# Kernel tuning notes

Measured on AMD Instinct MI355X. Metric: run time of the kernel, lower is better.

The kernel has to match this reference:

```python
import jax, jax.numpy as jnp
import numpy as np

B, NE, DE = 4096, 64, 96
NA, NACT = 8, 16
DH, NH, OD = 256, 4, 64
HD = DH // NH


def setup_inputs() -> dict:
    key = jax.random.key(0)
    ks = jax.random.split(key, 16)
    s = 0.02
    entities = jax.random.normal(ks[0], (B, NE, DE), jnp.float32)
    entity_mask = jax.random.randint(ks[1], (B, NE), 0, 2, jnp.int32)
    obs_mask = jax.random.randint(ks[2], (B, NE, NE), 0, 2, jnp.int32)
    act_ids = jax.random.randint(ks[3], (B, NA), 0, NACT)
    actions_onehot = jax.nn.one_hot(act_ids, NACT, dtype=jnp.float32)
    return {
        "entities": entities,
        "entity_mask": entity_mask,
        "obs_mask": obs_mask,
        "actions_onehot": actions_onehot,
        "We": jax.random.normal(ks[4], (DE, DH), jnp.float32) * s,
        "be": jnp.zeros((DH,), jnp.float32),
        "Wa": jax.random.normal(ks[5], (NACT, DH), jnp.float32) * s,
        "Win": jax.random.normal(ks[6], (DH, 3 * DH), jnp.float32) * s,
        "Wout": jax.random.normal(ks[7], (DH, DH), jnp.float32) * s,
        "bout": jnp.zeros((DH,), jnp.float32),
        "Wm1": jax.random.normal(ks[8], (DH, DH), jnp.float32) * s,
        "bm1": jnp.zeros((DH,), jnp.float32),
        "Wm2": jax.random.normal(ks[9], (DH, OD), jnp.float32) * s,
        "bm2": jnp.zeros((OD,), jnp.float32),
        "Wl1": jax.random.normal(ks[10], (DH, DH), jnp.float32) * s,
        "bl1": jnp.zeros((DH,), jnp.float32),
        "Wl2": jax.random.normal(ks[11], (DH, OD), jnp.float32) * s,
        "bl2": jnp.zeros((OD,), jnp.float32),
    }


def reference(entities, entity_mask, obs_mask, actions_onehot,
              We, be, Wa, Win, Wout, bout,
              Wm1, bm1, Wm2, bm2, Wl1, bl1, Wl2, bl2):
    # entity encode + action embed, scattered into first NA entity slots
    he = entities @ We + be                      # [B, NE, DH]
    ha = actions_onehot @ Wa                     # [B, NA, DH]
    ha_pad = jnp.zeros_like(he).at[:, :NA].set(ha)
    x = jax.nn.relu(he + ha_pad)                 # [B, NE, DH]

    # multi-head attention: NA agent queries attend to NE entities
    qkv = x @ Win                                # [B, NE, 3*DH]
    q, k, v = jnp.split(qkv, 3, axis=-1)
    q = q[:, :NA].reshape(B, NA, NH, HD)
    k = k.reshape(B, NE, NH, HD)
    v = v.reshape(B, NE, NH, HD)
    logits = jnp.einsum('bqhd,bkhd->bhqk', q, k) / jnp.sqrt(jnp.float32(HD))
    pre = obs_mask[:, :NA, :NE].astype(bool)[:, None, :, :]  # [B,1,NA,NE]
    logits = jnp.where(pre, -jnp.inf, logits)
    w = jax.nn.softmax(logits, axis=-1)
    w = jnp.where(jnp.isnan(w), 0.0, w)          # fully-masked rows -> 0
    attn = jnp.einsum('bhqk,bkhd->bqhd', w, v).reshape(B, NA, DH)
    attn = attn @ Wout + bout
    post = entity_mask[:, :NA].astype(bool)[..., None]  # [B, NA, 1]
    hidden = jax.nn.relu(jnp.where(post, 0.0, attn))

    mean = jax.nn.relu(hidden @ Wm1 + bm1) @ Wm2 + bm2
    logvar = jnp.clip(jax.nn.relu(hidden @ Wl1 + bl1) @ Wl2 + bl2, -10.0, 0.0)
    return mean, logvar
```

## Files before the change

### kernel.cpp

```cpp
#include <hip/hip_runtime.h>
#include <hip/hip_bf16.h>
#include <math.h>

typedef __attribute__((ext_vector_type(8))) short short8;
typedef __attribute__((ext_vector_type(4))) float f32x4;
typedef __attribute__((ext_vector_type(2))) unsigned int uint2v;

#define DEVINL static __device__ __forceinline__

static constexpr int NBLK = 2048;

static constexpr int WE_OFF  = 0;
static constexpr int WQ_OFF  = 24576;
static constexpr int WKT_OFF = 90112;
static constexpr int WV_OFF  = 155648;
static constexpr int WO_OFF  = 221184;
static constexpr int WM1_OFF = 286720;
static constexpr int WM2_OFF = 352256;
static constexpr int WL1_OFF = 368640;
static constexpr int WL2_OFF = 434176;

static constexpr int XOFF   = 0;
static constexpr int WLOFF  = 0;
static constexpr int ATOFF  = 8192;
static constexpr int HOFF   = 16384;
static constexpr int M1OFF  = 24576;
static constexpr int L1OFF  = 32768;
static constexpr int XTOFF  = 65536;
static constexpr int EOFF   = 131072;
static constexpr int TOFF   = 131072;
static constexpr int WXOFF  = 131072;
static constexpr int ACTOFF = 155648;
static constexpr int QOFF   = 155648;
static constexpr int LDS_BYTES = 163840;

DEVINL unsigned short f2bf(float f) {
  union { float f; unsigned u; } x; x.f = f;
  unsigned r = x.u + 0x7fffu + ((x.u >> 16) & 1u);
  return (unsigned short)(r >> 16);
}

DEVINL f32x4 mfma(short8 a, short8 b, f32x4 c) {
  return __builtin_amdgcn_mfma_f32_16x16x32_bf16(a, b, c, 0, 0, 0);
}

DEVINL short8 ldfrag(const unsigned short* wf, int off, int nt, int kt, int nkt, int lane) {
  return *(const short8*)(wf + off + ((nt * nkt + kt) << 9) + (lane << 3));
}

__global__ __launch_bounds__(512) void prep_kernel(
    const float* We, const float* Win, const float* Wout, const float* Wm1,
    const float* Wm2, const float* Wl1, const float* Wl2, unsigned short* wf) {
  const int m = blockIdx.y;
  const int idx = blockIdx.x * 512 + threadIdx.x;
  if (m == 2) {
    if (idx >= 65536) return;
    const int h = idx >> 14, d = (idx >> 6) & 255, hd = idx & 63;
    const float v = Win[(long)d * 768 + 256 + h * 64 + hd];
    const int kt = hd >> 5, gg = (hd >> 3) & 3, j = hd & 7;
    wf[WKT_OFF + (((h * 16 + (d >> 4)) * 2 + kt) << 9) + (gg * 16 + (d & 15)) * 8 + j] =
        f2bf(v);
    return;
  }
  const int Ks[9]  = {96, 256, 0, 256, 256, 256, 256, 256, 256};
  const int Ns[9]  = {256, 256, 0, 256, 256, 256, 64, 256, 64};
  const int ld_[9] = {256, 768, 0, 768, 256, 256, 64, 256, 64};
  const int co_[9] = {0, 0, 0, 512, 0, 0, 0, 0, 0};
  const int off[9] = {WE_OFF, WQ_OFF, 0, WV_OFF, WO_OFF, WM1_OFF, WM2_OFF, WL1_OFF, WL2_OFF};
  const float* S[9] = {We, Win, Win, Win, Wout, Wm1, Wm2, Wl1, Wl2};
  const int K = Ks[m], N = Ns[m];
  if (idx >= K * N) return;
  const int row = idx / N, col = idx - row * N;
  const float v = S[m][(long)row * ld_[m] + co_[m] + col];
  const int nkt = K >> 5;
  wf[off[m] + ((((col >> 4) * nkt) + (row >> 5)) << 9) +
     ((((row >> 3) & 3) << 4) + (col & 15)) * 8 + (row & 7)] = f2bf(v);
}

__global__ __launch_bounds__(1024, 4) void fused_kernel(
    const float* __restrict__ entities, const int* __restrict__ entity_mask,
    const int* __restrict__ obs_mask, const float* __restrict__ acts,
    const float* __restrict__ Wa, const float* __restrict__ be,
    const float* __restrict__ bout, const float* __restrict__ bm1,
    const float* __restrict__ bm2, const float* __restrict__ bl1,
    const float* __restrict__ bl2, const unsigned short* __restrict__ wf,
    float* __restrict__ out) {
  extern __shared__ char sm[];
  const int tid = threadIdx.x;
  const int w = tid >> 6, lane = tid & 63;
  const int g = lane >> 4, c = lane & 15;
  const int ig0 = blockIdx.x * 2;

  {
    const int it = tid >> 9, i = tid & 511;
    const int row = i >> 3, seg = i & 7;
    const float* src = entities + (long)(ig0 + it) * 6144 + row * 96 + seg * 12;
    const int ebase = EOFF + it * 12288 + row * 192;
    const int sw = (row & 3) << 4;
#pragma unroll
    for (int p = 0; p < 3; ++p) {
      float4 f = *(const float4*)(src + p * 4);
      uint2v u;
      u.x = f2bf(f.x) | ((unsigned)f2bf(f.y) << 16);
      u.y = f2bf(f.z) | ((unsigned)f2bf(f.w) << 16);
      *(uint2v*)(sm + ebase + ((seg * 24 + p * 8) ^ sw)) = u;
    }
    if (tid < 16) {
      const float* oh = acts + ((long)(ig0 + (tid >> 3)) * 8 + (tid & 7)) * 16;
      int id = 0;
#pragma unroll
      for (int a = 0; a < 16; ++a) if (oh[a] > 0.5f) id = a;
      ((int*)(sm + ACTOFF))[tid] = id;
    }
  }
  __syncthreads();

  {
    f32x4 acc[2][4] = {};
#pragma unroll
    for (int kt = 0; kt < 3; ++kt) {
      short8 b = ldfrag(wf, WE_OFF, w, kt, 3, lane);
#pragma unroll
      for (int it = 0; it < 2; ++it)
#pragma unroll
        for (int mt = 0; mt < 4; ++mt) {
          const int row = mt * 16 + c;
          short8 a = *(const short8*)(sm + EOFF + it * 12288 + row * 192 +
                                      ((kt * 64 + g * 16) ^ ((row & 3) << 4)));
          acc[it][mt] = mfma(a, b, acc[it][mt]);
        }
    }
    const int col = w * 16 + c;
    const float bev = be[col];
#pragma unroll
    for (int it = 0; it < 2; ++it)
#pragma unroll
      for (int mt = 0; mt < 4; ++mt) {
        float vv[4];
#pragma unroll
        for (int r = 0; r < 4; ++r) {
          const int row = mt * 16 + g * 4 + r;
          float v = acc[it][mt][r] + bev;
          if (row < 8) {
            int id = ((const int*)(sm + ACTOFF))[it * 8 + row];
            v += Wa[id * 256 + col];
          }
          v = fmaxf(v, 0.f);
          vv[r] = v;
          *(unsigned short*)(sm + XOFF + it * 32768 + row * 512 +
                             ((col * 2) ^ ((row & 7) << 4))) = f2bf(v);
        }
        uint2v u;
        u.x = f2bf(vv[0]) | ((unsigned)f2bf(vv[1]) << 16);
        u.y = f2bf(vv[2]) | ((unsigned)f2bf(vv[3]) << 16);
        *(uint2v*)(sm + XTOFF + it * 32768 + col * 128 +
                   ((mt * 32 + g * 8) ^ ((col & 7) << 4))) = u;
      }
  }
  __syncthreads();

  {
    f32x4 qa = {0.f, 0.f, 0.f, 0.f};
#pragma unroll
    for (int kt = 0; kt < 8; ++kt) {
      short8 b = ldfrag(wf, WQ_OFF, w, kt, 8, lane);
      short8 a = *(const short8*)(sm + XOFF + (c >> 3) * 32768 + (c & 7) * 512 +
                                  ((kt * 64 + g * 16) ^ ((c & 7) << 4)));
      qa = mfma(a, b, qa);
    }
#pragma unroll
    for (int r = 0; r < 4; ++r) {
      const int qq = g * 4 + r;
      *(unsigned short*)(sm + QOFF + qq * 512 +
                         (((w * 16 + c) * 2) ^ ((qq & 7) << 4))) = f2bf(qa[r]);
    }
  }
  __syncthreads();

  {
    const int h = w >> 2, dq = w & 3;
    f32x4 ta[4] = {};
#pragma unroll
    for (int kt = 0; kt < 2; ++kt) {
      short8 a = *(const short8*)(sm + QOFF + c * 512 +
                                  ((h * 128 + kt * 64 + g * 16) ^ ((c & 7) << 4)));
#pragma unroll
      for (int n = 0; n < 4; ++n) {
        short8 b = ldfrag(wf, WKT_OFF, h * 16 + dq * 4 + n, kt, 2, lane);
        ta[n] = mfma(a, b, ta[n]);
      }
    }
    __syncthreads();
#pragma unroll
    for (int n = 0; n < 4; ++n)
#pragma unroll
      for (int r = 0; r < 4; ++r) {
        const int qq = g * 4 + r;
        const int col = (dq * 4 + n) * 16 + c;
        *(unsigned short*)(sm + TOFF + h * 8192 + qq * 512 +
                           ((col * 2) ^ ((qq & 7) << 4))) = f2bf(ta[n][r]);
      }
  }
  __syncthreads();

  {
    const int it = (w >> 2) & 1, h = w & 3;
    float wvals[4][4];
    f32x4 lac[4] = {};
    if (w < 8) {
#pragma unroll
      for (int kt = 0; kt < 8; ++kt) {
        short8 a = *(const short8*)(sm + TOFF + h * 8192 + (it * 8 + (c & 7)) * 512 +
                                    ((kt * 64 + g * 16) ^ ((c & 7) << 4)));
#pragma unroll
        for (int nt = 0; nt < 4; ++nt) {
          const int key = nt * 16 + c;
          short8 b = *(const short8*)(sm + XOFF + it * 32768 + key * 512 +
                                      ((kt * 64 + g * 16) ^ ((key & 7) << 4)));
          lac[nt] = mfma(a, b, lac[nt]);
        }
      }
      if (g < 2) {
        const int* obs = obs_mask + (long)(ig0 + it) * 4096;
#pragma unroll
        for (int r = 0; r < 4; ++r) {
          const int qi = g * 4 + r;
          float vals[4];
#pragma unroll
          for (int nt = 0; nt < 4; ++nt) {
            int msk = obs[qi * 64 + nt * 16 + c];
            vals[nt] = msk ? -INFINITY : lac[nt][r] * 0.125f;
          }
          float mx = fmaxf(fmaxf(vals[0], vals[1]), fmaxf(vals[2], vals[3]));
#pragma unroll
          for (int d = 1; d < 16; d <<= 1) mx = fmaxf(mx, __shfl_xor(mx, d, 64));
          float s = 0.f;
#pragma unroll
          for (int nt = 0; nt < 4; ++nt) {
            float e = (mx == -INFINITY) ? 0.f : expf(vals[nt] - mx);
            vals[nt] = e; s += e;
          }
#pragma unroll
          for (int d = 1; d < 16; d <<= 1) s += __shfl_xor(s, d, 64);
          const float inv = (s > 0.f) ? 1.f / s : 0.f;
#pragma unroll
          for (int nt = 0; nt < 4; ++nt) wvals[r][nt] = vals[nt] * inv;
        }
      }
    }
    __syncthreads();
    if (w < 8 && g < 2) {
#pragma unroll
      for (int r = 0; r < 4; ++r) {
        const int qi = g * 4 + r;
#pragma unroll
        for (int nt = 0; nt < 4; ++nt) {
          const int key = nt * 16 + c;
          *(unsigned short*)(sm + WLOFF + ((it * 4 + h) * 8 + qi) * 128 +
                             ((key * 2) ^ ((qi & 7) << 4))) = f2bf(wvals[r][nt]);
        }
      }
    }
  }
  __syncthreads();

  {
    const int it = w >> 3, h = (w >> 1) & 3, dh = w & 1;
    f32x4 xa[8] = {};
#pragma unroll
    for (int kt = 0; kt < 2; ++kt) {
      short8 a = *(const short8*)(sm + WLOFF + ((it * 4 + h) * 8 + (c & 7)) * 128 +
                                  ((kt * 64 + g * 16) ^ ((c & 7) << 4)));
#pragma unroll
      for (int n = 0; n < 8; ++n) {
        const int d = dh * 128 + n * 16 + c;
        short8 b = *(const short8*)(sm + XTOFF + it * 32768 + d * 128 +
                                    ((kt * 64 + g * 16) ^ ((d & 7) << 4)));
        xa[n] = mfma(a, b, xa[n]);
      }
    }
    if (g < 2) {
#pragma unroll
      for (int n = 0; n < 8; ++n)
#pragma unroll
        for (int r = 0; r < 4; ++r) {
          const int qq = it * 8 + g * 4 + r;
          const int col = h * 256 + dh * 128 + n * 16 + c;
          *(unsigned short*)(sm + WXOFF + qq * 2048 +
                             ((col * 2) ^ ((qq & 7) << 4))) = f2bf(xa[n][r]);
        }
    }
  }
  __syncthreads();

  {
    const int h = w >> 2, n = w & 3;
    f32x4 aac = {0.f, 0.f, 0.f, 0.f};
#pragma unroll
    for (int kt = 0; kt < 8; ++kt) {
      short8 a = *(const short8*)(sm + WXOFF + c * 2048 +
                                  ((h * 512 + kt * 64 + g * 16) ^ ((c & 7) << 4)));
      short8 b = ldfrag(wf, WV_OFF, h * 4 + n, kt, 8, lane);
      aac = mfma(a, b, aac);
    }
#pragma unroll
    for (int r = 0; r < 4; ++r) {
      const int qq = g * 4 + r;
      const int col = (h * 4 + n) * 16 + c;
      *(unsigned short*)(sm + ATOFF + qq * 512 +
                         ((col * 2) ^ ((qq & 7) << 4))) = f2bf(aac[r]);
    }
  }
  __syncthreads();

  {
    f32x4 hc = {0.f, 0.f, 0.f, 0.f};
#pragma unroll
    for (int kt = 0; kt < 8; ++kt) {
      short8 a = *(const short8*)(sm + ATOFF + c * 512 +
                                  ((kt * 64 + g * 16) ^ ((c & 7) << 4)));
      short8 b = ldfrag(wf, WO_OFF, w, kt, 8, lane);
      hc = mfma(a, b, hc);
    }
    const int col = w * 16 + c;
    const float bo = bout[col];
#pragma unroll
    for (int r = 0; r < 4; ++r) {
      const int qq = g * 4 + r;
      const int em = entity_mask[(long)(ig0 + (qq >> 3)) * 64 + (qq & 7)];
      float v = hc[r] + bo;
      v = em ? 0.f : fmaxf(v, 0.f);
      *(unsigned short*)(sm + HOFF + qq * 512 + ((col * 2) ^ ((qq & 7) << 4))) = f2bf(v);
    }
  }
  __syncthreads();

  {
    const int which = w >> 3, np = w & 7;
    const int woff = which ? WL1_OFF : WM1_OFF;
    const float* bias = which ? bl1 : bm1;
    const int base = which ? L1OFF : M1OFF;
    f32x4 mc[2] = {};
#pragma unroll
    for (int kt = 0; kt < 8; ++kt) {
      short8 a = *(const short8*)(sm + HOFF + c * 512 +
                                  ((kt * 64 + g * 16) ^ ((c & 7) << 4)));
      short8 b0 = ldfrag(wf, woff, np * 2, kt, 8, lane);
      short8 b1 = ldfrag(wf, woff, np * 2 + 1, kt, 8, lane);
      mc[0] = mfma(a, b0, mc[0]);
      mc[1] = mfma(a, b1, mc[1]);
    }
#pragma unroll
    for (int n = 0; n < 2; ++n) {
      const int col = (np * 2 + n) * 16 + c;
      const float bv = bias[col];
#pragma unroll
      for (int r = 0; r < 4; ++r) {
        const int qq = g * 4 + r;
        float v = fmaxf(mc[n][r] + bv, 0.f);
        *(unsigned short*)(sm + base + qq * 512 + ((col * 2) ^ ((qq & 7) << 4))) = f2bf(v);
      }
    }
  }
  __syncthreads();

  if (w < 8) {
    const int which = w >> 2, nt = w & 3;
    const int woff = which ? WL2_OFF : WM2_OFF;
    const int base = which ? L1OFF : M1OFF;
    const float* bias = which ? bl2 : bm2;
    f32x4 oc = {0.f, 0.f, 0.f, 0.f};
#pragma unroll
    for (int kt = 0; kt < 8; ++kt) {
      short8 a = *(const short8*)(sm + base + c * 512 +
                                  ((kt * 64 + g * 16) ^ ((c & 7) << 4)));
      short8 b = ldfrag(wf, woff, nt, kt, 8, lane);
      oc = mfma(a, b, oc);
    }
    const float bv = bias[nt * 16 + c];
#pragma unroll
    for (int r = 0; r < 4; ++r) {
      const int qq = g * 4 + r;
      float v = oc[r] + bv;
      if (which) v = fminf(fmaxf(v, -10.f), 0.f);
      out[(long)which * 2097152 + (long)(ig0 + (qq >> 3)) * 512 + (qq & 7) * 64 +
          nt * 16 + c] = v;
    }
  }
}

extern "C" void kernel_launch(void* const* d_in, const int* in_sizes, int n_in,
                              void* d_out, int out_size, void* d_ws, size_t ws_size,
                              hipStream_t stream) {
  const float* entities    = (const float*)d_in[0];
  const int*   entity_mask = (const int*)d_in[1];
  const int*   obs_mask    = (const int*)d_in[2];
  const float* acts        = (const float*)d_in[3];
  const float* We   = (const float*)d_in[4];
  const float* be   = (const float*)d_in[5];
  const float* Wa   = (const float*)d_in[6];
  const float* Win  = (const float*)d_in[7];
  const float* Wout = (const float*)d_in[8];
  const float* bout = (const float*)d_in[9];
  const float* Wm1  = (const float*)d_in[10];
  const float* bm1  = (const float*)d_in[11];
  const float* Wm2  = (const float*)d_in[12];
  const float* bm2  = (const float*)d_in[13];
  const float* Wl1  = (const float*)d_in[14];
  const float* bl1  = (const float*)d_in[15];
  const float* Wl2  = (const float*)d_in[16];
  const float* bl2  = (const float*)d_in[17];
  unsigned short* wf = (unsigned short*)d_ws;

  prep_kernel<<<dim3(128, 9), 512, 0, stream>>>(We, Win, Wout, Wm1, Wm2, Wl1, Wl2, wf);

  hipFuncSetAttribute((const void*)fused_kernel,
                      hipFuncAttributeMaxDynamicSharedMemorySize, LDS_BYTES);
  fused_kernel<<<NBLK, 1024, LDS_BYTES, stream>>>(
      entities, entity_mask, obs_mask, acts, Wa, be, bout, bm1, bm2, bl1, bl2,
      wf, (float*)d_out);
}
```

Before: 352.6 us.

## Split fused kernel into front/back kernels with precomputed Wq·Wkᵀ per head

Replaces the single fused kernel with a front kernel (one batch item per block, attention via a precomputed per-head Wq·Wkᵀ product, so keys are scored directly against x) and a back kernel that batches 64 query rows per block for the output projection and MLP heads. Attention output goes through a bf16 global buffer between the kernels. V is computed per item and the weight-fragment prep is restructured. The aim is to cut per-item Q/K projection work, raise MFMA M-utilisation in the MLP stages and shrink LDS so more blocks fit per CU. In exchange it adds a global round trip and extra launches, and __expf slightly changes numerics.

```diff
diff --git a/kernel.cpp b/kernel.cpp
--- a/kernel.cpp
+++ b/kernel.cpp
@@ -8,31 +8,27 @@
 
 #define DEVINL static __device__ __forceinline__
 
-static constexpr int NBLK = 2048;
 
 static constexpr int WE_OFF  = 0;
-static constexpr int WQ_OFF  = 24576;
-static constexpr int WKT_OFF = 90112;
-static constexpr int WV_OFF  = 155648;
-static constexpr int WO_OFF  = 221184;
-static constexpr int WM1_OFF = 286720;
-static constexpr int WM2_OFF = 352256;
-static constexpr int WL1_OFF = 368640;
-static constexpr int WL2_OFF = 434176;
+static constexpr int MQK_OFF = 24576;
+static constexpr int WV_OFF  = 286720;
+static constexpr int WO_OFF  = 352256;
+static constexpr int WM1_OFF = 417792;
+static constexpr int WM2_OFF = 483328;
+static constexpr int WL1_OFF = 499712;
+static constexpr int WL2_OFF = 565248;
+static constexpr int ATTN_OFF = 581632;
 
 static constexpr int XOFF   = 0;
-static constexpr int WLOFF  = 0;
-static constexpr int ATOFF  = 8192;
-static constexpr int HOFF   = 16384;
-static constexpr int M1OFF  = 24576;
-static constexpr int L1OFF  = 32768;
-static constexpr int XTOFF  = 65536;
-static constexpr int EOFF   = 131072;
-static constexpr int TOFF   = 131072;
-static constexpr int WXOFF  = 131072;
-static constexpr int ACTOFF = 155648;
-static constexpr int QOFF   = 155648;
-static constexpr int LDS_BYTES = 163840;
+static constexpr int VTOFF  = 32768;
+static constexpr int EOFF   = 65536;
+static constexpr int ACTOFF = 77824;
+static constexpr int LDS_F  = 81920;
+
+static constexpr int B_AT = 0;
+static constexpr int B_H  = 32768;
+static constexpr int B_EM = 65536;
+static constexpr int LDS_B = 65792;
 
 DEVINL unsigned short f2bf(float f) {
   union { float f; unsigned u; } x; x.f = f;
@@ -48,54 +44,90 @@
   return *(const short8*)(wf + off + ((nt * nkt + kt) << 9) + (lane << 3));
 }
 
-__global__ __launch_bounds__(512) void prep_kernel(
+__global__ __launch_bounds__(512) void prep_frag(
     const float* We, const float* Win, const float* Wout, const float* Wm1,
     const float* Wm2, const float* Wl1, const float* Wl2, unsigned short* wf) {
   const int m = blockIdx.y;
-  const int idx = blockIdx.x * 512 + threadIdx.x;
-  if (m == 2) {
-    if (idx >= 65536) return;
-    const int h = idx >> 14, d = (idx >> 6) & 255, hd = idx & 63;
-    const float v = Win[(long)d * 768 + 256 + h * 64 + hd];
-    const int kt = hd >> 5, gg = (hd >> 3) & 3, j = hd & 7;
-    wf[WKT_OFF + (((h * 16 + (d >> 4)) * 2 + kt) << 9) + (gg * 16 + (d & 15)) * 8 + j] =
-        f2bf(v);
-    return;
-  }
-  const int Ks[9]  = {96, 256, 0, 256, 256, 256, 256, 256, 256};
-  const int Ns[9]  = {256, 256, 0, 256, 256, 256, 64, 256, 64};
-  const int ld_[9] = {256, 768, 0, 768, 256, 256, 64, 256, 64};
-  const int co_[9] = {0, 0, 0, 512, 0, 0, 0, 0, 0};
-  const int off[9] = {WE_OFF, WQ_OFF, 0, WV_OFF, WO_OFF, WM1_OFF, WM2_OFF, WL1_OFF, WL2_OFF};
-  const float* S[9] = {We, Win, Win, Win, Wout, Wm1, Wm2, Wl1, Wl2};
-  const int K = Ks[m], N = Ns[m];
-  if (idx >= K * N) return;
-  const int row = idx / N, col = idx - row * N;
-  const float v = S[m][(long)row * ld_[m] + co_[m] + col];
-  const int nkt = K >> 5;
-  wf[off[m] + ((((col >> 4) * nkt) + (row >> 5)) << 9) +
-     ((((row >> 3) & 3) << 4) + (col & 15)) * 8 + (row & 7)] = f2bf(v);
-}
-
-__global__ __launch_bounds__(1024, 4) void fused_kernel(
-    const float* __restrict__ entities, const int* __restrict__ entity_mask,
-    const int* __restrict__ obs_mask, const float* __restrict__ acts,
-    const float* __restrict__ Wa, const float* __restrict__ be,
-    const float* __restrict__ bout, const float* __restrict__ bm1,
-    const float* __restrict__ bm2, const float* __restrict__ bl1,
-    const float* __restrict__ bl2, const unsigned short* __restrict__ wf,
-    float* __restrict__ out) {
+  const int Ks[7]  = {96, 256, 256, 256, 256, 256, 256};
+  const int Ns[7]  = {256, 256, 256, 256, 64, 256, 64};
+  const int ld_[7] = {256, 768, 256, 256, 64, 256, 64};
+  const int co_[7] = {0, 512, 0, 0, 0, 0, 0};
+  const int off[7] = {WE_OFF, WV_OFF, WO_OFF, WM1_OFF, WM2_OFF, WL1_OFF, WL2_OFF};
+  const float* S[7] = {We, Win, Wout, Wm1, Wm2, Wl1, Wl2};
+  const int K = Ks[m], N = Ns[m], nkt = K >> 5;
+  const int fid = blockIdx.x * 512 + threadIdx.x;
+  if (fid >= (N >> 4) * nkt * 64) return;
+  const int lane = fid & 63;
+  const int kt = (fid >> 6) % nkt;
+  const int nt = fid / (nkt << 6);
+  const int row0 = kt * 32 + ((lane >> 4) << 3);
+  const int col = nt * 16 + (lane & 15);
+  const float* sp = S[m] + (long)row0 * ld_[m] + co_[m] + col;
+  const int ld = ld_[m];
+  short8 s;
+#pragma unroll
+  for (int j = 0; j < 8; ++j) s[j] = (short)f2bf(sp[j * ld]);
+  *(short8*)(wf + off[m] + fid * 8) = s;
+}
+
+__global__ __launch_bounds__(1024) void prep_mqk(const float* __restrict__ Win,
+                                                 unsigned short* __restrict__ wf) {
+  __shared__ char smq[65536];
+  const int h = blockIdx.x;
+  const int tid = threadIdx.x;
+  const int w = tid >> 6, lane = tid & 63, g = lane >> 4, c = lane & 15;
+  {
+    const int d = tid >> 2, hd0 = (tid & 3) * 16;
+    const int sw = (d & 7) << 4;
+#pragma unroll
+    for (int mat = 0; mat < 2; ++mat) {
+      const float* srcp = Win + (long)d * 768 + mat * 256 + h * 64 + hd0;
+      short8 s0, s1;
+#pragma unroll
+      for (int j = 0; j < 8; ++j) s0[j] = (short)f2bf(srcp[j]);
+#pragma unroll
+      for (int j = 0; j < 8; ++j) s1[j] = (short)f2bf(srcp[8 + j]);
+      char* base = smq + mat * 32768 + d * 128;
+      *(short8*)(base + ((hd0 * 2) ^ sw)) = s0;
+      *(short8*)(base + ((hd0 * 2 + 16) ^ sw)) = s1;
+    }
+  }
+  __syncthreads();
+#pragma unroll 4
+  for (int mt = 0; mt < 16; ++mt) {
+    f32x4 acc = {0.f, 0.f, 0.f, 0.f};
+#pragma unroll
+    for (int kt = 0; kt < 2; ++kt) {
+      const int ra = mt * 16 + c;
+      short8 a = *(const short8*)(smq + ra * 128 + ((kt * 64 + g * 16) ^ ((ra & 7) << 4)));
+      const int rb = w * 16 + c;
+      short8 b = *(const short8*)(smq + 32768 + rb * 128 + ((kt * 64 + g * 16) ^ ((rb & 7) << 4)));
+      acc = mfma(a, b, acc);
+    }
+#pragma unroll
+    for (int r = 0; r < 4; ++r) {
+      const int d1 = mt * 16 + g * 4 + r;
+      wf[MQK_OFF + h * 65536 + ((w * 8 + (d1 >> 5)) << 9) +
+         ((((d1 >> 3) & 3) << 4) + c) * 8 + (d1 & 7)] = f2bf(acc[r]);
+    }
+  }
+}
+
+__global__ __launch_bounds__(512, 4) void front_kernel(
+    const float* __restrict__ entities, const int* __restrict__ obs_mask,
+    const float* __restrict__ acts, const float* __restrict__ Wa,
+    const float* __restrict__ be, const unsigned short* __restrict__ wf,
+    unsigned short* __restrict__ attn_g) {
   extern __shared__ char sm[];
   const int tid = threadIdx.x;
   const int w = tid >> 6, lane = tid & 63;
   const int g = lane >> 4, c = lane & 15;
-  const int ig0 = blockIdx.x * 2;
-
-  {
-    const int it = tid >> 9, i = tid & 511;
-    const int row = i >> 3, seg = i & 7;
-    const float* src = entities + (long)(ig0 + it) * 6144 + row * 96 + seg * 12;
-    const int ebase = EOFF + it * 12288 + row * 192;
+  const long ig = blockIdx.x;
+
+  {
+    const int row = tid >> 3, seg = tid & 7;
+    const float* src = entities + ig * 6144 + row * 96 + seg * 12;
+    const int ebase = EOFF + row * 192;
     const int sw = (row & 3) << 4;
 #pragma unroll
     for (int p = 0; p < 3; ++p) {
@@ -105,8 +137,8 @@
       u.y = f2bf(f.z) | ((unsigned)f2bf(f.w) << 16);
       *(uint2v*)(sm + ebase + ((seg * 24 + p * 8) ^ sw)) = u;
     }
-    if (tid < 16) {
-      const float* oh = acts + ((long)(ig0 + (tid >> 3)) * 8 + (tid & 7)) * 16;
+    if (tid < 8) {
+      const float* oh = acts + (ig * 8 + tid) * 16;
       int id = 0;
 #pragma unroll
       for (int a = 0; a < 16; ++a) if (oh[a] > 0.5f) id = a;
@@ -116,112 +148,90 @@
   __syncthreads();
 
   {
-    f32x4 acc[2][4] = {};
+    f32x4 acc[4][2] = {};
 #pragma unroll
     for (int kt = 0; kt < 3; ++kt) {
-      short8 b = ldfrag(wf, WE_OFF, w, kt, 3, lane);
-#pragma unroll
-      for (int it = 0; it < 2; ++it)
-#pragma unroll
-        for (int mt = 0; mt < 4; ++mt) {
-          const int row = mt * 16 + c;
-          short8 a = *(const short8*)(sm + EOFF + it * 12288 + row * 192 +
-                                      ((kt * 64 + g * 16) ^ ((row & 3) << 4)));
-          acc[it][mt] = mfma(a, b, acc[it][mt]);
-        }
-    }
-    const int col = w * 16 + c;
-    const float bev = be[col];
-#pragma unroll
-    for (int it = 0; it < 2; ++it)
+      short8 b0 = ldfrag(wf, WE_OFF, 2 * w, kt, 3, lane);
+      short8 b1 = ldfrag(wf, WE_OFF, 2 * w + 1, kt, 3, lane);
 #pragma unroll
       for (int mt = 0; mt < 4; ++mt) {
-        float vv[4];
+        const int row = mt * 16 + c;
+        short8 a = *(const short8*)(sm + EOFF + row * 192 +
+                                    ((kt * 64 + g * 16) ^ ((row & 3) << 4)));
+        acc[mt][0] = mfma(a, b0, acc[mt][0]);
+        acc[mt][1] = mfma(a, b1, acc[mt][1]);
+      }
+    }
+#pragma unroll
+    for (int n = 0; n < 2; ++n) {
+      const int col = (2 * w + n) * 16 + c;
+      const float bev = be[col];
+#pragma unroll
+      for (int mt = 0; mt < 4; ++mt)
 #pragma unroll
         for (int r = 0; r < 4; ++r) {
           const int row = mt * 16 + g * 4 + r;
-          float v = acc[it][mt][r] + bev;
+          float v = acc[mt][n][r] + bev;
           if (row < 8) {
-            int id = ((const int*)(sm + ACTOFF))[it * 8 + row];
+            int id = ((const int*)(sm + ACTOFF))[row];
             v += Wa[id * 256 + col];
           }
           v = fmaxf(v, 0.f);
-          vv[r] = v;
-          *(unsigned short*)(sm + XOFF + it * 32768 + row * 512 +
+          *(unsigned short*)(sm + XOFF + row * 512 +
                              ((col * 2) ^ ((row & 7) << 4))) = f2bf(v);
         }
-        uint2v u;
-        u.x = f2bf(vv[0]) | ((unsigned)f2bf(vv[1]) << 16);
-        u.y = f2bf(vv[2]) | ((unsigned)f2bf(vv[3]) << 16);
-        *(uint2v*)(sm + XTOFF + it * 32768 + col * 128 +
-                   ((mt * 32 + g * 8) ^ ((col & 7) << 4))) = u;
-      }
-  }
-  __syncthreads();
-
-  {
-    f32x4 qa = {0.f, 0.f, 0.f, 0.f};
-#pragma unroll
-    for (int kt = 0; kt < 8; ++kt) {
-      short8 b = ldfrag(wf, WQ_OFF, w, kt, 8, lane);
-      short8 a = *(const short8*)(sm + XOFF + (c >> 3) * 32768 + (c & 7) * 512 +
+    }
+  }
+  __syncthreads();
+
+  {
+    const int h = w >> 1;
+    f32x4 ta[8] = {};
+#pragma unroll
+    for (int kt = 0; kt < 8; ++kt) {
+      short8 a = *(const short8*)(sm + XOFF + (c & 7) * 512 +
                                   ((kt * 64 + g * 16) ^ ((c & 7) << 4)));
-      qa = mfma(a, b, qa);
-    }
-#pragma unroll
-    for (int r = 0; r < 4; ++r) {
-      const int qq = g * 4 + r;
-      *(unsigned short*)(sm + QOFF + qq * 512 +
-                         (((w * 16 + c) * 2) ^ ((qq & 7) << 4))) = f2bf(qa[r]);
-    }
-  }
-  __syncthreads();
-
-  {
-    const int h = w >> 2, dq = w & 3;
-    f32x4 ta[4] = {};
-#pragma unroll
-    for (int kt = 0; kt < 2; ++kt) {
-      short8 a = *(const short8*)(sm + QOFF + c * 512 +
-                                  ((h * 128 + kt * 64 + g * 16) ^ ((c & 7) << 4)));
-#pragma unroll
-      for (int n = 0; n < 4; ++n) {
-        short8 b = ldfrag(wf, WKT_OFF, h * 16 + dq * 4 + n, kt, 2, lane);
+#pragma unroll
+      for (int n = 0; n < 8; ++n) {
+        short8 b = ldfrag(wf, MQK_OFF + h * 65536, (w & 1) * 8 + n, kt, 8, lane);
         ta[n] = mfma(a, b, ta[n]);
       }
     }
-    __syncthreads();
-#pragma unroll
-    for (int n = 0; n < 4; ++n)
-#pragma unroll
-      for (int r = 0; r < 4; ++r) {
-        const int qq = g * 4 + r;
-        const int col = (dq * 4 + n) * 16 + c;
-        *(unsigned short*)(sm + TOFF + h * 8192 + qq * 512 +
-                           ((col * 2) ^ ((qq & 7) << 4))) = f2bf(ta[n][r]);
-      }
-  }
-  __syncthreads();
-
-  {
-    const int it = (w >> 2) & 1, h = w & 3;
+    if (g < 2) {
+#pragma unroll
+      for (int n = 0; n < 8; ++n) {
+        const int nt = (w & 1) * 8 + n;
+#pragma unroll
+        for (int r = 0; r < 4; ++r) {
+          const int q = g * 4 + r;
+          const int col = nt * 16 + c;
+          *(unsigned short*)(sm + EOFF + h * 4096 + q * 512 +
+                             ((col * 2) ^ (q << 4))) = f2bf(ta[n][r]);
+        }
+      }
+    }
+  }
+  __syncthreads();
+
+  {
     float wvals[4][4];
-    f32x4 lac[4] = {};
-    if (w < 8) {
+    const int h = w;
+    if (w < 4) {
+      f32x4 lac[4] = {};
 #pragma unroll
       for (int kt = 0; kt < 8; ++kt) {
-        short8 a = *(const short8*)(sm + TOFF + h * 8192 + (it * 8 + (c & 7)) * 512 +
+        short8 a = *(const short8*)(sm + EOFF + h * 4096 + (c & 7) * 512 +
                                     ((kt * 64 + g * 16) ^ ((c & 7) << 4)));
 #pragma unroll
         for (int nt = 0; nt < 4; ++nt) {
           const int key = nt * 16 + c;
-          short8 b = *(const short8*)(sm + XOFF + it * 32768 + key * 512 +
+          short8 b = *(const short8*)(sm + XOFF + key * 512 +
                                       ((kt * 64 + g * 16) ^ ((key & 7) << 4)));
           lac[nt] = mfma(a, b, lac[nt]);
         }
       }
       if (g < 2) {
-        const int* obs = obs_mask + (long)(ig0 + it) * 4096;
+        const int* obs = obs_mask + ig * 4096;
 #pragma unroll
         for (int r = 0; r < 4; ++r) {
           const int qi = g * 4 + r;
@@ -237,7 +247,7 @@
           float s = 0.f;
 #pragma unroll
           for (int nt = 0; nt < 4; ++nt) {
-            float e = (mx == -INFINITY) ? 0.f : expf(vals[nt] - mx);
+            float e = (mx == -INFINITY) ? 0.f : __expf(vals[nt] - mx);
             vals[nt] = e; s += e;
           }
 #pragma unroll
@@ -249,143 +259,250 @@
       }
     }
     __syncthreads();
-    if (w < 8 && g < 2) {
+    if (w < 4 && g < 2) {
 #pragma unroll
       for (int r = 0; r < 4; ++r) {
         const int qi = g * 4 + r;
 #pragma unroll
         for (int nt = 0; nt < 4; ++nt) {
           const int key = nt * 16 + c;
-          *(unsigned short*)(sm + WLOFF + ((it * 4 + h) * 8 + qi) * 128 +
-                             ((key * 2) ^ ((qi & 7) << 4))) = f2bf(wvals[r][nt]);
-        }
-      }
-    }
-  }
-  __syncthreads();
-
-  {
-    const int it = w >> 3, h = (w >> 1) & 3, dh = w & 1;
-    f32x4 xa[8] = {};
-#pragma unroll
-    for (int kt = 0; kt < 2; ++kt) {
-      short8 a = *(const short8*)(sm + WLOFF + ((it * 4 + h) * 8 + (c & 7)) * 128 +
-                                  ((kt * 64 + g * 16) ^ ((c & 7) << 4)));
-#pragma unroll
-      for (int n = 0; n < 8; ++n) {
-        const int d = dh * 128 + n * 16 + c;
-        short8 b = *(const short8*)(sm + XTOFF + it * 32768 + d * 128 +
-                                    ((kt * 64 + g * 16) ^ ((d & 7) << 4)));
-        xa[n] = mfma(a, b, xa[n]);
+          *(unsigned short*)(sm + EOFF + (h * 8 + qi) * 128 +
+                             ((key * 2) ^ (qi << 4))) = f2bf(wvals[r][nt]);
+        }
+      }
+    }
+  }
+
+  {
+    f32x4 acc[4][2] = {};
+#pragma unroll
+    for (int kt = 0; kt < 8; ++kt) {
+      short8 b0 = ldfrag(wf, WV_OFF, 2 * w, kt, 8, lane);
+      short8 b1 = ldfrag(wf, WV_OFF, 2 * w + 1, kt, 8, lane);
+#pragma unroll
+      for (int mt = 0; mt < 4; ++mt) {
+        const int row = mt * 16 + c;
+        short8 a = *(const short8*)(sm + XOFF + row * 512 +
+                                    ((kt * 64 + g * 16) ^ ((row & 7) << 4)));
+        acc[mt][0] = mfma(a, b0, acc[mt][0]);
+        acc[mt][1] = mfma(a, b1, acc[mt][1]);
+      }
+    }
+#pragma unroll
+    for (int n = 0; n < 2; ++n) {
+      const int col = (2 * w + n) * 16 + c;
+#pragma unroll
+      for (int mt = 0; mt < 4; ++mt) {
+        unsigned long long pk = 0;
+#pragma unroll
+        for (int r = 0; r < 4; ++r)
+          pk |= (unsigned long long)f2bf(acc[mt][n][r]) << (16 * r);
+        *(unsigned long long*)(sm + VTOFF + col * 128 +
+                               ((mt * 32 + g * 8) ^ ((col & 7) << 4))) = pk;
+      }
+    }
+  }
+  __syncthreads();
+
+  {
+    f32x4 aac[2] = {};
+#pragma unroll
+    for (int e = 0; e < 2; ++e) {
+      const int tt = w * 2 + e, h = tt >> 2, n2 = tt & 3;
+#pragma unroll
+      for (int kt = 0; kt < 2; ++kt) {
+        short8 a = *(const short8*)(sm + EOFF + h * 1024 + (c & 7) * 128 +
+                                    ((kt * 64 + g * 16) ^ ((c & 7) << 4)));
+        const int vrow = h * 64 + n2 * 16 + c;
+        short8 b = *(const short8*)(sm + VTOFF + vrow * 128 +
+                                    ((kt * 64 + g * 16) ^ ((vrow & 7) << 4)));
+        aac[e] = mfma(a, b, aac[e]);
       }
     }
     if (g < 2) {
 #pragma unroll
-      for (int n = 0; n < 8; ++n)
-#pragma unroll
-        for (int r = 0; r < 4; ++r) {
-          const int qq = it * 8 + g * 4 + r;
-          const int col = h * 256 + dh * 128 + n * 16 + c;
-          *(unsigned short*)(sm + WXOFF + qq * 2048 +
-                             ((col * 2) ^ ((qq & 7) << 4))) = f2bf(xa[n][r]);
-        }
-    }
-  }
-  __syncthreads();
-
-  {
-    const int h = w >> 2, n = w & 3;
-    f32x4 aac = {0.f, 0.f, 0.f, 0.f};
-#pragma unroll
-    for (int kt = 0; kt < 8; ++kt) {
-      short8 a = *(const short8*)(sm + WXOFF + c * 2048 +
-                                  ((h * 512 + kt * 64 + g * 16) ^ ((c & 7) << 4)));
-      short8 b = ldfrag(wf, WV_OFF, h * 4 + n, kt, 8, lane);
-      aac = mfma(a, b, aac);
-    }
-#pragma unroll
-    for (int r = 0; r < 4; ++r) {
-      const int qq = g * 4 + r;
-      const int col = (h * 4 + n) * 16 + c;
-      *(unsigned short*)(sm + ATOFF + qq * 512 +
-                         ((col * 2) ^ ((qq & 7) << 4))) = f2bf(aac[r]);
-    }
-  }
-  __syncthreads();
-
-  {
-    f32x4 hc = {0.f, 0.f, 0.f, 0.f};
-#pragma unroll
-    for (int kt = 0; kt < 8; ++kt) {
-      short8 a = *(const short8*)(sm + ATOFF + c * 512 +
-                                  ((kt * 64 + g * 16) ^ ((c & 7) << 4)));
-      short8 b = ldfrag(wf, WO_OFF, w, kt, 8, lane);
-      hc = mfma(a, b, hc);
-    }
-    const int col = w * 16 + c;
-    const float bo = bout[col];
-#pragma unroll
-    for (int r = 0; r < 4; ++r) {
-      const int qq = g * 4 + r;
-      const int em = entity_mask[(long)(ig0 + (qq >> 3)) * 64 + (qq & 7)];
-      float v = hc[r] + bo;
-      v = em ? 0.f : fmaxf(v, 0.f);
-      *(unsigned short*)(sm + HOFF + qq * 512 + ((col * 2) ^ ((qq & 7) << 4))) = f2bf(v);
-    }
-  }
-  __syncthreads();
-
-  {
-    const int which = w >> 3, np = w & 7;
-    const int woff = which ? WL1_OFF : WM1_OFF;
-    const float* bias = which ? bl1 : bm1;
-    const int base = which ? L1OFF : M1OFF;
-    f32x4 mc[2] = {};
-#pragma unroll
-    for (int kt = 0; kt < 8; ++kt) {
-      short8 a = *(const short8*)(sm + HOFF + c * 512 +
-                                  ((kt * 64 + g * 16) ^ ((c & 7) << 4)));
-      short8 b0 = ldfrag(wf, woff, np * 2, kt, 8, lane);
-      short8 b1 = ldfrag(wf, woff, np * 2 + 1, kt, 8, lane);
-      mc[0] = mfma(a, b0, mc[0]);
-      mc[1] = mfma(a, b1, mc[1]);
+      for (int e = 0; e < 2; ++e) {
+        const int tt = w * 2 + e, h = tt >> 2, n2 = tt & 3;
+#pragma unroll
+        for (int r = 0; r < 4; ++r) {
+          const int q = g * 4 + r;
+          const int col = h * 64 + n2 * 16 + c;
+          attn_g[(ig * 8 + q) * 256 + (col ^ (q << 3))] = f2bf(aac[e][r]);
+        }
+      }
+    }
+  }
+}
+
+__global__ __launch_bounds__(512, 4) void back_kernel(
+    const int* __restrict__ entity_mask, const float* __restrict__ bout,
+    const float* __restrict__ bm1, const float* __restrict__ bm2,
+    const float* __restrict__ bl1, const float* __restrict__ bl2,
+    const unsigned short* __restrict__ wf, const unsigned short* __restrict__ attn_g,
+    float* __restrict__ out) {
+  extern __shared__ char sm[];
+  const int tid = threadIdx.x;
+  const int w = tid >> 6, lane = tid & 63;
+  const int g = lane >> 4, c = lane & 15;
+  const long blk = blockIdx.x;
+
+  {
+    const uint4* src = (const uint4*)(attn_g + blk * 16384);
+#pragma unroll
+    for (int itr = 0; itr < 4; ++itr)
+      *(uint4*)(sm + B_AT + itr * 8192 + tid * 16) = src[itr * 512 + tid];
+    if (tid < 64)
+      ((int*)(sm + B_EM))[tid] = entity_mask[(blk * 8 + (tid >> 3)) * 64 + (tid & 7)];
+  }
+  __syncthreads();
+
+  {
+    f32x4 acc[4][2] = {};
+#pragma unroll
+    for (int kt = 0; kt < 8; ++kt) {
+      short8 b0 = ldfrag(wf, WO_OFF, 2 * w, kt, 8, lane);
+      short8 b1 = ldfrag(wf, WO_OFF, 2 * w + 1, kt, 8, lane);
+#pragma unroll
+      for (int mt = 0; mt < 4; ++mt) {
+        const int row = mt * 16 + c;
+        short8 a = *(const short8*)(sm + B_AT + row * 512 +
+                                    ((kt * 64 + g * 16) ^ ((row & 7) << 4)));
+        acc[mt][0] = mfma(a, b0, acc[mt][0]);
+        acc[mt][1] = mfma(a, b1, acc[mt][1]);
+      }
     }
 #pragma unroll
     for (int n = 0; n < 2; ++n) {
-      const int col = (np * 2 + n) * 16 + c;
-      const float bv = bias[col];
+      const int col = (2 * w + n) * 16 + c;
+      const float bo = bout[col];
+#pragma unroll
+      for (int mt = 0; mt < 4; ++mt)
+#pragma unroll
+        for (int r = 0; r < 4; ++r) {
+          const int row = mt * 16 + g * 4 + r;
+          const int em = ((const int*)(sm + B_EM))[row];
+          float v = acc[mt][n][r] + bo;
+          v = em ? 0.f : fmaxf(v, 0.f);
+          *(unsigned short*)(sm + B_H + row * 512 +
+                             ((col * 2) ^ ((row & 7) << 4))) = f2bf(v);
+        }
+    }
+  }
+  __syncthreads();
+
+  {
+    f32x4 acc[4][2] = {};
+#pragma unroll
+    for (int kt = 0; kt < 8; ++kt) {
+      short8 b0 = ldfrag(wf, WM1_OFF, 2 * w, kt, 8, lane);
+      short8 b1 = ldfrag(wf, WM1_OFF, 2 * w + 1, kt, 8, lane);
+#pragma unroll
+      for (int mt = 0; mt < 4; ++mt) {
+        const int row = mt * 16 + c;
+        short8 a = *(const short8*)(sm + B_H + row * 512 +
+                                    ((kt * 64 + g * 16) ^ ((row & 7) << 4)));
+        acc[mt][0] = mfma(a, b0, acc[mt][0]);
+        acc[mt][1] = mfma(a, b1, acc[mt][1]);
+      }
+    }
+#pragma unroll
+    for (int n = 0; n < 2; ++n) {
+      const int col = (2 * w + n) * 16 + c;
+      const float bv = bm1[col];
+#pragma unroll
+      for (int mt = 0; mt < 4; ++mt)
+#pragma unroll
+        for (int r = 0; r < 4; ++r) {
+          const int row = mt * 16 + g * 4 + r;
+          float v = fmaxf(acc[mt][n][r] + bv, 0.f);
+          *(unsigned short*)(sm + B_AT + row * 512 +
+                             ((col * 2) ^ ((row & 7) << 4))) = f2bf(v);
+        }
+    }
+  }
+  __syncthreads();
+
+  {
+    const int mh = w >> 2, nt = w & 3;
+    f32x4 acc[2] = {};
+#pragma unroll
+    for (int kt = 0; kt < 8; ++kt) {
+      short8 b = ldfrag(wf, WM2_OFF, nt, kt, 8, lane);
+#pragma unroll
+      for (int m2 = 0; m2 < 2; ++m2) {
+        const int row = (mh * 2 + m2) * 16 + c;
+        short8 a = *(const short8*)(sm + B_AT + row * 512 +
+                                    ((kt * 64 + g * 16) ^ ((row & 7) << 4)));
+        acc[m2] = mfma(a, b, acc[m2]);
+      }
+    }
+    const float bv = bm2[nt * 16 + c];
+#pragma unroll
+    for (int m2 = 0; m2 < 2; ++m2)
 #pragma unroll
       for (int r = 0; r < 4; ++r) {
-        const int qq = g * 4 + r;
-        float v = fmaxf(mc[n][r] + bv, 0.f);
-        *(unsigned short*)(sm + base + qq * 512 + ((col * 2) ^ ((qq & 7) << 4))) = f2bf(v);
-      }
-    }
-  }
-  __syncthreads();
-
-  if (w < 8) {
-    const int which = w >> 2, nt = w & 3;
-    const int woff = which ? WL2_OFF : WM2_OFF;
-    const int base = which ? L1OFF : M1OFF;
-    const float* bias = which ? bl2 : bm2;
-    f32x4 oc = {0.f, 0.f, 0.f, 0.f};
-#pragma unroll
-    for (int kt = 0; kt < 8; ++kt) {
-      short8 a = *(const short8*)(sm + base + c * 512 +
-                                  ((kt * 64 + g * 16) ^ ((c & 7) << 4)));
-      short8 b = ldfrag(wf, woff, nt, kt, 8, lane);
-      oc = mfma(a, b, oc);
-    }
-    const float bv = bias[nt * 16 + c];
-#pragma unroll
-    for (int r = 0; r < 4; ++r) {
-      const int qq = g * 4 + r;
-      float v = oc[r] + bv;
-      if (which) v = fminf(fmaxf(v, -10.f), 0.f);
-      out[(long)which * 2097152 + (long)(ig0 + (qq >> 3)) * 512 + (qq & 7) * 64 +
-          nt * 16 + c] = v;
-    }
+        const int row = (mh * 2 + m2) * 16 + g * 4 + r;
+        out[(blk * 8 + (row >> 3)) * 512 + (row & 7) * 64 + nt * 16 + c] = acc[m2][r] + bv;
+      }
+  }
+  __syncthreads();
+
+  {
+    f32x4 acc[4][2] = {};
+#pragma unroll
+    for (int kt = 0; kt < 8; ++kt) {
+      short8 b0 = ldfrag(wf, WL1_OFF, 2 * w, kt, 8, lane);
+      short8 b1 = ldfrag(wf, WL1_OFF, 2 * w + 1, kt, 8, lane);
+#pragma unroll
+      for (int mt = 0; mt < 4; ++mt) {
+        const int row = mt * 16 + c;
+        short8 a = *(const short8*)(sm + B_H + row * 512 +
+                                    ((kt * 64 + g * 16) ^ ((row & 7) << 4)));
+        acc[mt][0] = mfma(a, b0, acc[mt][0]);
+        acc[mt][1] = mfma(a, b1, acc[mt][1]);
+      }
+    }
+#pragma unroll
+    for (int n = 0; n < 2; ++n) {
+      const int col = (2 * w + n) * 16 + c;
+      const float bv = bl1[col];
+#pragma unroll
+      for (int mt = 0; mt < 4; ++mt)
+#pragma unroll
+        for (int r = 0; r < 4; ++r) {
+          const int row = mt * 16 + g * 4 + r;
+          float v = fmaxf(acc[mt][n][r] + bv, 0.f);
+          *(unsigned short*)(sm + B_AT + row * 512 +
+                             ((col * 2) ^ ((row & 7) << 4))) = f2bf(v);
+        }
+    }
+  }
+  __syncthreads();
+
+  {
+    const int mh = w >> 2, nt = w & 3;
+    f32x4 acc[2] = {};
+#pragma unroll
+    for (int kt = 0; kt < 8; ++kt) {
+      short8 b = ldfrag(wf, WL2_OFF, nt, kt, 8, lane);
+#pragma unroll
+      for (int m2 = 0; m2 < 2; ++m2) {
+        const int row = (mh * 2 + m2) * 16 + c;
+        short8 a = *(const short8*)(sm + B_AT + row * 512 +
+                                    ((kt * 64 + g * 16) ^ ((row & 7) << 4)));
+        acc[m2] = mfma(a, b, acc[m2]);
+      }
+    }
+    const float bv = bl2[nt * 16 + c];
+#pragma unroll
+    for (int m2 = 0; m2 < 2; ++m2)
+#pragma unroll
+      for (int r = 0; r < 4; ++r) {
+        const int row = (mh * 2 + m2) * 16 + g * 4 + r;
+        float v = acc[m2][r] + bv;
+        v = fminf(fmaxf(v, -10.f), 0.f);
+        out[2097152 + (blk * 8 + (row >> 3)) * 512 + (row & 7) * 64 + nt * 16 + c] = v;
+      }
   }
 }
 
@@ -411,12 +528,17 @@
   const float* Wl2  = (const float*)d_in[16];
   const float* bl2  = (const float*)d_in[17];
   unsigned short* wf = (unsigned short*)d_ws;
-
-  prep_kernel<<<dim3(128, 9), 512, 0, stream>>>(We, Win, Wout, Wm1, Wm2, Wl1, Wl2, wf);
-
-  hipFuncSetAttribute((const void*)fused_kernel,
-                      hipFuncAttributeMaxDynamicSharedMemorySize, LDS_BYTES);
-  fused_kernel<<<NBLK, 1024, LDS_BYTES, stream>>>(
-      entities, entity_mask, obs_mask, acts, Wa, be, bout, bm1, bm2, bl1, bl2,
-      wf, (float*)d_out);
-}
+  unsigned short* attn_g = wf + ATTN_OFF;
+
+  prep_frag<<<dim3(16, 7), 512, 0, stream>>>(We, Win, Wout, Wm1, Wm2, Wl1, Wl2, wf);
+  prep_mqk<<<4, 1024, 0, stream>>>(Win, wf);
+
+  hipFuncSetAttribute((const void*)front_kernel,
+                      hipFuncAttributeMaxDynamicSharedMemorySize, LDS_F);
+  hipFuncSetAttribute((const void*)back_kernel,
+                      hipFuncAttributeMaxDynamicSharedMemorySize, LDS_B);
+
+  front_kernel<<<4096, 512, LDS_F, stream>>>(entities, obs_mask, acts, Wa, be, wf, attn_g);
+  back_kernel<<<512, 512, LDS_B, stream>>>(entity_mask, bout, bm1, bm2, bl1, bl2,
+                                           wf, attn_g, (float*)d_out);
+}
```

Result: slower. 388.0 us (+10.0%).
